# Kernel tuning notes

Hardware: AMD Instinct MI355X
Metric: run time of the kernel (lower is better)

Reference implementation:

```python
import jax, jax.numpy as jnp
import numpy as np

N_INTERP = 5      # `count = 5` in the original
MAXDIS = 0.001    # threshold default (thresholding/list-build is data-dependent; see notes)


def _pairwise_edge_cdis(recon, gt):
    """Fused, vectorized version of the original double Python loop.

    recon: [B, N, D] keypoints; gt: [B, M, D].
    Returns cdis [B, P] where P = N*(N-1)/2 lower-triangular pairs (i>j),
    cdis[b, p] = mean over 5 interpolated points of min squared distance to gt[b].
    """
    B, N, D = recon.shape
    ii, jj = jnp.tril_indices(N, -1)                 # P pairs, i > j (same order as the loops)
    P = ii.shape[0]
    start = recon[:, ii, :]                          # [B, P, D]
    end = recon[:, jj, :]                            # [B, P, D]
    f = jnp.linspace(0.0, 1.0, N_INTERP, dtype=recon.dtype).reshape(1, 1, N_INTERP, 1)
    # K = start * f_interp + end * (1 - f_interp)   -> [B, P, 5, D]
    K = start[:, :, None, :] * f + end[:, :, None, :] * (1.0 - f)
    Kf = K.reshape(B, P * N_INTERP, D)               # flatten pairs x interp
    diff = Kf[:, :, None, :] - gt[:, None, :, :]     # [B, P*5, M, D]
    dist = jnp.sum(diff * diff, axis=3)              # [B, P*5, M] squared distances
    dmin = jnp.min(dist, axis=2)                     # min over gt points (dist1 in original)
    cdis = jnp.mean(dmin.reshape(B, P, N_INTERP), axis=2)  # mean over 5 interp points
    return cdis                                      # [B, P]


def setup_inputs() -> dict:
    key = jax.random.key(0)
    k1, k2 = jax.random.split(key)
    return {
        "recon_points": jax.random.uniform(k1, (4, 64, 3), dtype=jnp.float32),
        "gt_points": jax.random.uniform(k2, (4, 2048, 3), dtype=jnp.float32),
    }


def reference(recon_points, gt_points):
    # Dense, fixed-shape equivalent of compute_edge_distance: the per-(batch, pair)
    # chamfer distance. The original thresholds cdis < maxdis and builds a python
    # dict of edges; that is a trivial host-side post-process of this tensor.
    return _pairwise_edge_cdis(recon_points, gt_points)
```

## Files before the change

kernel.cpp:

```cpp
#include <hip/hip_runtime.h>
#include <hip/hip_bf16.h>
#include <math.h>

#define BATCH 4
#define NPTS 64
#define MGT 2048
#define NPAIR 2016
#define PPW 2
#define THREADS 1024
#define WAVES_PER_BLOCK 16
#define PAIRS_PER_BLOCK (WAVES_PER_BLOCK * PPW)
#define BLOCKS_PER_BATCH (NPAIR / PAIRS_PER_BLOCK)

__global__ __launch_bounds__(THREADS)
void edge_cdis_kernel(const float* __restrict__ recon,
                      const float* __restrict__ gt,
                      float* __restrict__ out) {
    __shared__ float4 gts4[MGT];

    const int tid  = threadIdx.x;
    const int wib  = tid >> 6;
    const int lane = tid & 63;

    const int b     = blockIdx.x / BLOCKS_PER_BATCH;
    const int pbase = (blockIdx.x % BLOCKS_PER_BATCH) * PAIRS_PER_BLOCK;

    const float* __restrict__ gtb = gt + b * (MGT * 3);
    #pragma unroll
    for (int p = tid; p < MGT; p += THREADS) {
        const float gx = gtb[p * 3 + 0];
        const float gy = gtb[p * 3 + 1];
        const float gz = gtb[p * 3 + 2];
        float4 v;
        v.x = -gx; v.y = -gy; v.z = -gz;
        v.w = 0.5f * fmaf(gz, gz, fmaf(gy, gy, gx * gx));
        gts4[p] = v;
    }
    __syncthreads();

    const float* __restrict__ rb = recon + b * (NPTS * 3);

    float ex[PPW], ey[PPW], ez[PPW];
    float ux[PPW], uy[PPW], uz[PPW];
    float e2[PPW], eu[PPW], c_[PPW];
    int og[PPW];
    #pragma unroll
    for (int k = 0; k < PPW; ++k) {
        const int p = pbase + wib * PPW + k;
        og[k] = b * NPAIR + p;
        int i = (int)((1.0f + sqrtf(1.0f + 8.0f * (float)p)) * 0.5f);
        while (i * (i - 1) / 2 > p) --i;
        while ((i + 1) * i / 2 <= p) ++i;
        const int j = p - i * (i - 1) / 2;
        const float sx = rb[i * 3 + 0], sy = rb[i * 3 + 1], sz = rb[i * 3 + 2];
        ex[k] = rb[j * 3 + 0]; ey[k] = rb[j * 3 + 1]; ez[k] = rb[j * 3 + 2];
        ux[k] = sx - ex[k]; uy[k] = sy - ey[k]; uz[k] = sz - ez[k];
        e2[k] = ex[k]*ex[k] + ey[k]*ey[k] + ez[k]*ez[k];
        eu[k] = ex[k]*ux[k] + ey[k]*uy[k] + ez[k]*uz[k];
        c_[k] = ux[k]*ux[k] + uy[k]*uy[k] + uz[k]*uz[k];
    }

    float r[PPW][5];
    #pragma unroll
    for (int k = 0; k < PPW; ++k)
        #pragma unroll
        for (int t = 0; t < 5; ++t) r[k][t] = 3.4e38f;

    #pragma unroll 8
    for (int g = lane; g < MGT; g += 64) {
        const float4 gv = gts4[g];
        #pragma unroll
        for (int k = 0; k < PPW; ++k) {
            float T0 = fmaf(ex[k], gv.x, gv.w);
            T0 = fmaf(ey[k], gv.y, T0);
            T0 = fmaf(ez[k], gv.z, T0);
            float G = ux[k] * gv.x;
            G = fmaf(uy[k], gv.y, G);
            G = fmaf(uz[k], gv.z, G);
            r[k][0] = fminf(r[k][0], T0);
            r[k][1] = fminf(r[k][1], fmaf(0.25f, G, T0));
            r[k][2] = fminf(r[k][2], fmaf(0.50f, G, T0));
            r[k][3] = fminf(r[k][3], fmaf(0.75f, G, T0));
            r[k][4] = fminf(r[k][4], T0 + G);
        }
    }

    #pragma unroll
    for (int k = 0; k < PPW; ++k)
        #pragma unroll
        for (int t = 0; t < 5; ++t)
            #pragma unroll
            for (int off = 32; off >= 1; off >>= 1)
                r[k][t] = fminf(r[k][t], __shfl_xor(r[k][t], off, 64));

    if (lane == 0) {
        #pragma unroll
        for (int k = 0; k < PPW; ++k) {
            const float sr = r[k][0] + r[k][1] + r[k][2] + r[k][3] + r[k][4];
            out[og[k]] = 0.4f * sr + e2[k] + eu[k] + 0.375f * c_[k];
        }
    }
}

extern "C" void kernel_launch(void* const* d_in, const int* in_sizes, int n_in,
                              void* d_out, int out_size, void* d_ws, size_t ws_size,
                              hipStream_t stream) {
    const float* recon = (const float*)d_in[0];
    const float* gt    = (const float*)d_in[1];
    float* out = (float*)d_out;

    const int blocks = BATCH * BLOCKS_PER_BATCH;
    edge_cdis_kernel<<<blocks, THREADS, 0, stream>>>(recon, gt, out);
}
```

Measured before the change: 13.16 us.

## Assign pair chunks by triangular row and share start-point distances per wave

Each wave now handles 4 pairs, using 512-thread blocks instead of 1024. Pairs are mapped by complementary triangular rows (P+1 and 63-P, with row 32 split separately), which replaces the sqrt-based pair index recovery. When all of a wave's pairs share the same start point, the distance to the start point is computed once per gt point and reused for every pair. This cuts per-point arithmetic and doubles register reuse of each LDS gt load. The trade-off is half as many waves per block while each block still stages the full gt set into LDS.

```diff
diff --git a/kernel.cpp b/kernel.cpp
--- a/kernel.cpp
+++ b/kernel.cpp
@@ -6,11 +6,11 @@
 #define NPTS 64
 #define MGT 2048
 #define NPAIR 2016
-#define PPW 2
-#define THREADS 1024
-#define WAVES_PER_BLOCK 16
-#define PAIRS_PER_BLOCK (WAVES_PER_BLOCK * PPW)
-#define BLOCKS_PER_BATCH (NPAIR / PAIRS_PER_BLOCK)
+#define PPW 4
+#define THREADS 512
+#define WAVES_PER_BLOCK 8
+#define CHUNKS_PER_BLOCK WAVES_PER_BLOCK
+#define BLOCKS_PER_BATCH 63
 
 __global__ __launch_bounds__(THREADS)
 void edge_cdis_kernel(const float* __restrict__ recon,
@@ -22,8 +22,8 @@
     const int wib  = tid >> 6;
     const int lane = tid & 63;
 
-    const int b     = blockIdx.x / BLOCKS_PER_BATCH;
-    const int pbase = (blockIdx.x % BLOCKS_PER_BATCH) * PAIRS_PER_BLOCK;
+    const int b  = blockIdx.x / BLOCKS_PER_BATCH;
+    const int cb = (blockIdx.x % BLOCKS_PER_BATCH) * CHUNKS_PER_BLOCK + wib;
 
     const float* __restrict__ gtb = gt + b * (MGT * 3);
     #pragma unroll
@@ -38,26 +38,40 @@
     }
     __syncthreads();
 
+    int i_[PPW], j_[PPW];
+    if (cb >= 496) {
+        const int base = (cb - 496) * 4;
+        #pragma unroll
+        for (int k = 0; k < PPW; ++k) { i_[k] = 32; j_[k] = base + k; }
+    } else {
+        const int P = cb >> 4;
+        const int o = cb & 15;
+        const int a = P + 1;
+        const int bb = 63 - P;
+        const int slot = o * 4;
+        #pragma unroll
+        for (int k = 0; k < PPW; ++k) {
+            const int sk = slot + k;
+            i_[k] = (sk < a) ? a : bb;
+            j_[k] = (sk < a) ? sk : (sk - a);
+        }
+    }
+    const bool same_row = (i_[0] == i_[PPW - 1]);
+
     const float* __restrict__ rb = recon + b * (NPTS * 3);
 
     float ex[PPW], ey[PPW], ez[PPW];
-    float ux[PPW], uy[PPW], uz[PPW];
-    float e2[PPW], eu[PPW], c_[PPW];
-    int og[PPW];
+    float sx[PPW], sy[PPW], sz[PPW];
+    float cadd[PPW];
     #pragma unroll
     for (int k = 0; k < PPW; ++k) {
-        const int p = pbase + wib * PPW + k;
-        og[k] = b * NPAIR + p;
-        int i = (int)((1.0f + sqrtf(1.0f + 8.0f * (float)p)) * 0.5f);
-        while (i * (i - 1) / 2 > p) --i;
-        while ((i + 1) * i / 2 <= p) ++i;
-        const int j = p - i * (i - 1) / 2;
-        const float sx = rb[i * 3 + 0], sy = rb[i * 3 + 1], sz = rb[i * 3 + 2];
-        ex[k] = rb[j * 3 + 0]; ey[k] = rb[j * 3 + 1]; ez[k] = rb[j * 3 + 2];
-        ux[k] = sx - ex[k]; uy[k] = sy - ey[k]; uz[k] = sz - ez[k];
-        e2[k] = ex[k]*ex[k] + ey[k]*ey[k] + ez[k]*ez[k];
-        eu[k] = ex[k]*ux[k] + ey[k]*uy[k] + ez[k]*uz[k];
-        c_[k] = ux[k]*ux[k] + uy[k]*uy[k] + uz[k]*uz[k];
+        sx[k] = rb[i_[k] * 3 + 0]; sy[k] = rb[i_[k] * 3 + 1]; sz[k] = rb[i_[k] * 3 + 2];
+        ex[k] = rb[j_[k] * 3 + 0]; ey[k] = rb[j_[k] * 3 + 1]; ez[k] = rb[j_[k] * 3 + 2];
+        const float ux = sx[k] - ex[k], uy = sy[k] - ey[k], uz = sz[k] - ez[k];
+        const float e2 = ex[k]*ex[k] + ey[k]*ey[k] + ez[k]*ez[k];
+        const float eu = ex[k]*ux + ey[k]*uy + ez[k]*uz;
+        const float c  = ux*ux + uy*uy + uz*uz;
+        cadd[k] = e2 + eu + 0.375f * c;
     }
 
     float r[PPW][5];
@@ -65,23 +79,48 @@
     for (int k = 0; k < PPW; ++k)
         #pragma unroll
         for (int t = 0; t < 5; ++t) r[k][t] = 3.4e38f;
+    float r4s = 3.4e38f;
 
-    #pragma unroll 8
-    for (int g = lane; g < MGT; g += 64) {
-        const float4 gv = gts4[g];
-        #pragma unroll
-        for (int k = 0; k < PPW; ++k) {
-            float T0 = fmaf(ex[k], gv.x, gv.w);
-            T0 = fmaf(ey[k], gv.y, T0);
-            T0 = fmaf(ez[k], gv.z, T0);
-            float G = ux[k] * gv.x;
-            G = fmaf(uy[k], gv.y, G);
-            G = fmaf(uz[k], gv.z, G);
-            r[k][0] = fminf(r[k][0], T0);
-            r[k][1] = fminf(r[k][1], fmaf(0.25f, G, T0));
-            r[k][2] = fminf(r[k][2], fmaf(0.50f, G, T0));
-            r[k][3] = fminf(r[k][3], fmaf(0.75f, G, T0));
-            r[k][4] = fminf(r[k][4], T0 + G);
+    if (same_row) {
+        const float Sx = sx[0], Sy = sy[0], Sz = sz[0];
+        #pragma unroll 4
+        for (int g = lane; g < MGT; g += 64) {
+            const float4 gv = gts4[g];
+            float Ds = fmaf(Sx, gv.x, gv.w);
+            Ds = fmaf(Sy, gv.y, Ds);
+            Ds = fmaf(Sz, gv.z, Ds);
+            r4s = fminf(r4s, Ds);
+            #pragma unroll
+            for (int k = 0; k < PPW; ++k) {
+                float A = fmaf(ex[k], gv.x, gv.w);
+                A = fmaf(ey[k], gv.y, A);
+                A = fmaf(ez[k], gv.z, A);
+                const float G = Ds - A;
+                r[k][0] = fminf(r[k][0], A);
+                r[k][1] = fminf(r[k][1], fmaf(0.25f, G, A));
+                r[k][2] = fminf(r[k][2], fmaf(0.50f, G, A));
+                r[k][3] = fminf(r[k][3], fmaf(0.75f, G, A));
+            }
+        }
+    } else {
+        #pragma unroll 4
+        for (int g = lane; g < MGT; g += 64) {
+            const float4 gv = gts4[g];
+            #pragma unroll
+            for (int k = 0; k < PPW; ++k) {
+                float A = fmaf(ex[k], gv.x, gv.w);
+                A = fmaf(ey[k], gv.y, A);
+                A = fmaf(ez[k], gv.z, A);
+                float Ds = fmaf(sx[k], gv.x, gv.w);
+                Ds = fmaf(sy[k], gv.y, Ds);
+                Ds = fmaf(sz[k], gv.z, Ds);
+                const float G = Ds - A;
+                r[k][0] = fminf(r[k][0], A);
+                r[k][1] = fminf(r[k][1], fmaf(0.25f, G, A));
+                r[k][2] = fminf(r[k][2], fmaf(0.50f, G, A));
+                r[k][3] = fminf(r[k][3], fmaf(0.75f, G, A));
+                r[k][4] = fminf(r[k][4], Ds);
+            }
         }
     }
 
@@ -92,12 +131,17 @@
             #pragma unroll
             for (int off = 32; off >= 1; off >>= 1)
                 r[k][t] = fminf(r[k][t], __shfl_xor(r[k][t], off, 64));
+    #pragma unroll
+    for (int off = 32; off >= 1; off >>= 1)
+        r4s = fminf(r4s, __shfl_xor(r4s, off, 64));
 
     if (lane == 0) {
         #pragma unroll
         for (int k = 0; k < PPW; ++k) {
-            const float sr = r[k][0] + r[k][1] + r[k][2] + r[k][3] + r[k][4];
-            out[og[k]] = 0.4f * sr + e2[k] + eu[k] + 0.375f * c_[k];
+            const float r4 = same_row ? r4s : r[k][4];
+            const float sr = r[k][0] + r[k][1] + r[k][2] + r[k][3] + r4;
+            const int p = i_[k] * (i_[k] - 1) / 2 + j_[k];
+            out[b * NPAIR + p] = 0.4f * sr + cadd[k];
         }
     }
 }
```

Measured after the change: 14.92 us. 13.4% more time.
